# Performance work log

Hardware: AMD Instinct MI355X
Metric: run time of the kernel (lower is better)

The kernel has to match this reference:

```python
import jax, jax.numpy as jnp
import numpy as np

B, S, H, D = 1, 8192, 16, 128
BS = 64            # sparse_block_size
NB = S // BS       # 128 blocks
NUM_ORACLES = 32
ORACLE = S // NUM_ORACLES          # 256
LOCAL = ORACLE // BS               # 4 sliding-window blocks
PATTERN_ID = 0


def _build_block_pattern():
    """Block-level mask exactly as DKernelPredefinedSparseAttention.create_mask((0,))."""
    qb = np.arange(NB)[:, None]
    kb = np.arange(NB)[None, :]
    causal = qb >= kb
    window = (qb - kb) < LOCAL
    vert = np.zeros(NB, dtype=bool)
    real_col = int(PATTERN_ID * ORACLE + 0.5)
    vert[real_col // BS:(real_col + ORACLE) // BS] = True
    vert[0:1] = True
    mask = causal & (window | vert[None, :])
    kmax = int(mask.sum(axis=1).max())  # = 8 for this pattern
    kidx = np.zeros((NB, kmax), dtype=np.int32)
    kvalid = np.zeros((NB, kmax), dtype=bool)
    for i in range(NB):
        idx = np.nonzero(mask[i])[0]
        kidx[i, :len(idx)] = idx
        kvalid[i, :len(idx)] = True
    return kidx, kvalid


def setup_inputs() -> dict:
    key = jax.random.key(0)
    kq, kk, kv = jax.random.split(key, 3)
    q = jax.random.normal(kq, (B, S, H, D), dtype=jnp.float32)
    k = jax.random.normal(kk, (B, S, H, D), dtype=jnp.float32)
    v = jax.random.normal(kv, (B, S, H, D), dtype=jnp.float32)
    kidx_np, kvalid_np = _build_block_pattern()
    return {"q": q, "k": k, "v": v,
            "kidx": jnp.asarray(kidx_np), "kvalid": jnp.asarray(kvalid_np)}


def reference(q, k, v, kidx, kvalid):
    # q,k,v: [B,S,H,D] (bshd). kidx/kvalid: [NB, Kmax] active k-block ids per q-block.
    b, s, h, d = q.shape
    nb = s // BS
    kmax = kidx.shape[1]
    qb = q.reshape(b, nb, BS, h, d)
    kb = k.reshape(b, nb, BS, h, d)
    vb = v.reshape(b, nb, BS, h, d)
    # Gather only active k/v blocks -> [B, nb, Kmax, BS, H, D]
    kg = kb[:, kidx]
    vg = vb[:, kidx]
    scale = 1.0 / jnp.sqrt(jnp.float32(d))
    # [B, H, nb, BS(q), Kmax, BS(k)]
    scores = jnp.einsum('bqahd,bqkchd->bhqakc', qb, kg) * scale
    # element-level causal mask within the block pattern
    qpos = jnp.arange(nb)[:, None] * BS + jnp.arange(BS)[None, :]          # [nb, BS]
    kpos = kidx[..., None] * BS + jnp.arange(BS)[None, None, :]            # [nb, Kmax, BS]
    allow = (qpos[:, :, None, None] >= kpos[:, None, :, :]) & kvalid[:, None, :, None]
    scores = jnp.where(allow[None, None], scores, jnp.float32(-1e30))
    probs = jax.nn.softmax(scores.reshape(b, h, nb, BS, kmax * BS), axis=-1)
    probs = probs.reshape(scores.shape)
    out = jnp.einsum('bhqakc,bqkchd->bqahd', probs, vg)
    return out.reshape(b, s, h, d)
```

## Files before the change

### kernel.cpp

```cpp
#include <hip/hip_runtime.h>
#include <hip/hip_bf16.h>

#define HH 16
#define DD 128
#define NBQ 128
#define SS 8192

typedef __attribute__((ext_vector_type(4))) float f32x4;
typedef __attribute__((ext_vector_type(4))) short bf16x4;
typedef __attribute__((ext_vector_type(8))) short bf16x8;

__device__ __forceinline__ short f2bf_hw(float f) {
  __hip_bfloat16 b = __float2bfloat16(f);
  return __builtin_bit_cast(short, b);
}

__device__ __forceinline__ void gload_lds16(const void* g, void* l) {
  __builtin_amdgcn_global_load_lds(
      (const __attribute__((address_space(1))) void*)g,
      (__attribute__((address_space(3))) void*)l, 16, 0, 0);
}

__global__ __launch_bounds__(256)
void conv_vt2_kernel(const float* __restrict__ vg, unsigned short* __restrict__ vt) {
  __shared__ unsigned short tile[128 * 72];
  const int kb = blockIdx.x, h = blockIdx.y, tid = threadIdx.x;
  {
    const int r = tid >> 2, q = tid & 3;
    const float* vp = vg + ((size_t)(kb * 64 + r) * HH + h) * DD + q * 32;
    #pragma unroll
    for (int c = 0; c < 8; ++c) {
      f32x4 a = *(const f32x4*)(vp + c * 4);
      #pragma unroll
      for (int j = 0; j < 4; ++j)
        tile[(q * 32 + c * 4 + j) * 72 + r] = (unsigned short)f2bf_hw(a[j]);
    }
  }
  __syncthreads();
  const int d = tid >> 1, half = tid & 1;
  unsigned short* op = vt + ((size_t)(h * NBQ + kb) * 128 + d) * 64 + half * 32;
  #pragma unroll
  for (int j = 0; j < 4; ++j) {
    bf16x8 f;
    #pragma unroll
    for (int e = 0; e < 8; ++e) {
      const int p = half * 32 + j * 8 + e;
      const int key = ((p >> 2) & 3) * 16 + (p >> 4) * 4 + (p & 3);
      f[e] = (short)tile[d * 72 + key];
    }
    *(bf16x8*)(op + j * 8) = f;
  }
}

#define SWK(o) ((o) ^ ((((o) >> 8) & 7) << 4))
#define SWV(o) ((o) ^ ((((o) >> 7) & 7) << 4))

__global__ __launch_bounds__(512, 2)
void sparse_attn_v18(const float* __restrict__ qg_, const float* __restrict__ kg,
                     const unsigned short* __restrict__ vtbuf, float* __restrict__ outg) {
  extern __shared__ __align__(16) char lds[];

  const int bx   = blockIdx.x;
  const int w    = (bx & 7) * 128 + (bx >> 3);
  const int h    = w >> 6;
  const int qgrp = w & 63;
  const int tid  = threadIdx.x;
  const int wid  = tid >> 6;
  const int lane = tid & 63;
  const int l15  = lane & 15;
  const int lg   = lane >> 4;

  const int qlo  = qgrp * 2, qhi = qgrp * 2 + 1;
  const int qb_w = qlo + (wid >> 2);
  const int rib0 = (wid & 3) * 16;

  const int nv     = (qhi + 1 < 4) ? qhi + 1 : 4;
  const int wstart = (qlo - 3 > 4) ? qlo - 3 : 4;
  const int nw     = (qhi - wstart + 1 > 0) ? qhi - wstart + 1 : 0;
  const int nlist  = nv + nw;

  const float scale = 0.12752030522080552f;

  const int rowg = qgrp * 128 + (wid >> 2) * 64 + rib0;

  bf16x8 qa[4];
  {
    const float* qp = qg_ + ((size_t)(rowg + l15) * HH + h) * DD;
    #pragma unroll
    for (int kc = 0; kc < 4; ++kc) {
      const int d0 = kc * 32 + lg * 8;
      f32x4 a = *(const f32x4*)(qp + d0);
      f32x4 b = *(const f32x4*)(qp + d0 + 4);
      bf16x8 f;
      f[0] = f2bf_hw(a[0] * scale); f[1] = f2bf_hw(a[1] * scale);
      f[2] = f2bf_hw(a[2] * scale); f[3] = f2bf_hw(a[3] * scale);
      f[4] = f2bf_hw(b[0] * scale); f[5] = f2bf_hw(b[1] * scale);
      f[6] = f2bf_hw(b[2] * scale); f[7] = f2bf_hw(b[3] * scale);
      qa[kc] = f;
    }
  }

  f32x4 oa[8];
  #pragma unroll
  for (int i = 0; i < 8; ++i) oa[i] = (f32x4){0.f, 0.f, 0.f, 0.f};
  float mr = -1e30f;
  float lr = 0.f;

  const int kkey = tid >> 3;
  const int kd0  = (tid & 7) * 16;
  const int kob0 = SWK(tid * 32);
  const int kob1 = SWK(tid * 32 + 16);
  const char* vbase = (const char*)vtbuf + ((size_t)h * NBQ << 14);
  const int vo0 = wid * 1024 + lane * 16;

  {
    const float* kp = kg + (((size_t)(0 * 64 + kkey)) * HH + h) * DD + kd0;
    f32x4 ka = *(const f32x4*)(kp);
    f32x4 kb_ = *(const f32x4*)(kp + 4);
    f32x4 kc = *(const f32x4*)(kp + 8);
    f32x4 kd = *(const f32x4*)(kp + 12);
    bf16x8 w0, w1;
    w0[0] = f2bf_hw(ka[0]); w0[1] = f2bf_hw(ka[1]); w0[2] = f2bf_hw(ka[2]); w0[3] = f2bf_hw(ka[3]);
    w0[4] = f2bf_hw(kb_[0]); w0[5] = f2bf_hw(kb_[1]); w0[6] = f2bf_hw(kb_[2]); w0[7] = f2bf_hw(kb_[3]);
    w1[0] = f2bf_hw(kc[0]); w1[1] = f2bf_hw(kc[1]); w1[2] = f2bf_hw(kc[2]); w1[3] = f2bf_hw(kc[3]);
    w1[4] = f2bf_hw(kd[0]); w1[5] = f2bf_hw(kd[1]); w1[6] = f2bf_hw(kd[2]); w1[7] = f2bf_hw(kd[3]);
    *(bf16x8*)(lds + kob0) = w0;
    *(bf16x8*)(lds + kob1) = w1;
    #pragma unroll
    for (int p = 0; p < 2; ++p) {
      const int o = p * 8192 + vo0;
      gload_lds16(vbase + SWV(o), lds + 32768 + p * 8192 + wid * 1024);
    }
  }
  __syncthreads();

  for (int t = 0; t < nlist; ++t) {
    const int kb = (t < nv) ? t : (wstart + (t - nv));
    const bool valid = (kb <= qb_w) && ((qb_w - kb < 4) || (kb < 4));
    char* Kb = lds + (t & 1) * 16384;
    char* Vb = lds + 32768 + (t & 1) * 16384;
    const bool havenext = (t + 1 < nlist);
    const int kbn = havenext ? ((t + 1 < nv) ? (t + 1) : (wstart + (t + 1 - nv))) : 0;

    f32x4 ks0, ks1, ks2, ks3;
    if (havenext) {
      const float* kp = kg + (((size_t)(kbn * 64 + kkey)) * HH + h) * DD + kd0;
      ks0 = *(const f32x4*)(kp);
      ks1 = *(const f32x4*)(kp + 4);
      ks2 = *(const f32x4*)(kp + 8);
      ks3 = *(const f32x4*)(kp + 12);
      const char* vsrc = vbase + ((size_t)kbn << 14);
      char* Vd = lds + 32768 + ((t + 1) & 1) * 16384;
      #pragma unroll
      for (int p = 0; p < 2; ++p) {
        const int o = p * 8192 + vo0;
        gload_lds16(vsrc + SWV(o), Vd + p * 8192 + wid * 1024);
      }
    }

    f32x4 s[4];
    if (valid) {
      #pragma unroll
      for (int kt = 0; kt < 4; ++kt) s[kt] = (f32x4){0.f, 0.f, 0.f, 0.f};
      __builtin_amdgcn_s_setprio(1);
      #pragma unroll
      for (int kt = 0; kt < 4; ++kt) {
        const int key = kt * 16 + l15;
        #pragma unroll
        for (int kc = 0; kc < 4; ++kc) {
          const int off = (key * 256 + (kc * 32 + lg * 8) * 2) ^ ((key & 7) << 4);
          bf16x8 kf = *(const bf16x8*)(Kb + off);
          s[kt] = __builtin_amdgcn_mfma_f32_16x16x32_bf16(kf, qa[kc], s[kt], 0, 0, 0);
        }
      }
      __builtin_amdgcn_s_setprio(0);
    }

    if (havenext) {
      char* Kd = lds + ((t + 1) & 1) * 16384;
      bf16x8 w0, w1;
      w0[0] = f2bf_hw(ks0[0]); w0[1] = f2bf_hw(ks0[1]); w0[2] = f2bf_hw(ks0[2]); w0[3] = f2bf_hw(ks0[3]);
      w0[4] = f2bf_hw(ks1[0]); w0[5] = f2bf_hw(ks1[1]); w0[6] = f2bf_hw(ks1[2]); w0[7] = f2bf_hw(ks1[3]);
      w1[0] = f2bf_hw(ks2[0]); w1[1] = f2bf_hw(ks2[1]); w1[2] = f2bf_hw(ks2[2]); w1[3] = f2bf_hw(ks2[3]);
      w1[4] = f2bf_hw(ks3[0]); w1[5] = f2bf_hw(ks3[1]); w1[6] = f2bf_hw(ks3[2]); w1[7] = f2bf_hw(ks3[3]);
      *(bf16x8*)(Kd + kob0) = w0;
      *(bf16x8*)(Kd + kob1) = w1;
    }

    if (valid) {
      if (kb == qb_w) {
        const int rib = rib0 + l15;
        #pragma unroll
        for (int kt = 0; kt < 4; ++kt)
          #pragma unroll
          for (int r = 0; r < 4; ++r) {
            const int key = kt * 16 + lg * 4 + r;
            if (rib < key) s[kt][r] = -1e30f;
          }
      }

      {
        float a0 = fmaxf(fmaxf(s[0][0], s[0][1]), fmaxf(s[0][2], s[0][3]));
        float a1 = fmaxf(fmaxf(s[1][0], s[1][1]), fmaxf(s[1][2], s[1][3]));
        float a2 = fmaxf(fmaxf(s[2][0], s[2][1]), fmaxf(s[2][2], s[2][3]));
        float a3 = fmaxf(fmaxf(s[3][0], s[3][1]), fmaxf(s[3][2], s[3][3]));
        float lanemax = fmaxf(fmaxf(a0, a1), fmaxf(a2, a3));
        if (!__all(lanemax <= mr + 8.f)) {
          float mx = lanemax;
          mx = fmaxf(mx, __shfl_xor(mx, 16));
          mx = fmaxf(mx, __shfl_xor(mx, 32));
          const float mnew = fmaxf(mr, mx);
          const float sc = __builtin_amdgcn_exp2f(mr - mnew);
          lr *= sc;
          mr = mnew;
          const float s0 = __shfl(sc, lg * 4 + 0);
          const float s1 = __shfl(sc, lg * 4 + 1);
          const float s2 = __shfl(sc, lg * 4 + 2);
          const float s3 = __shfl(sc, lg * 4 + 3);
          #pragma unroll
          for (int nd = 0; nd < 8; ++nd) {
            oa[nd][0] *= s0; oa[nd][1] *= s1;
            oa[nd][2] *= s2; oa[nd][3] *= s3;
          }
        }
        float lsum = 0.f;
        #pragma unroll
        for (int kt = 0; kt < 4; ++kt)
          #pragma unroll
          for (int r = 0; r < 4; ++r) {
            const float p = __builtin_amdgcn_exp2f(s[kt][r] - mr);
            s[kt][r] = p;
            lsum += p;
          }
        lr += lsum;
      }

      bf16x4 pa[4];
      #pragma unroll
      for (int kt = 0; kt < 4; ++kt) {
        unsigned u0 = (unsigned)(unsigned short)f2bf_hw(s[kt][0]) |
                      ((unsigned)(unsigned short)f2bf_hw(s[kt][1]) << 16);
        unsigned u1 = (unsigned)(unsigned short)f2bf_hw(s[kt][2]) |
                      ((unsigned)(unsigned short)f2bf_hw(s[kt][3]) << 16);
        uint2 uu; uu.x = u0; uu.y = u1;
        pa[kt] = __builtin_bit_cast(bf16x4, uu);
      }

      __builtin_amdgcn_s_setprio(1);
      #pragma unroll
      for (int nd = 0; nd < 8; ++nd) {
        const int d = nd * 16 + l15;
        #pragma unroll
        for (int hb = 0; hb < 2; ++hb) {
          const int off = (d * 128 + lg * 32 + hb * 16) ^ ((d & 7) << 4);
          bf16x8 v2 = *(const bf16x8*)(Vb + off);
          bf16x4 vlo = __builtin_shufflevector(v2, v2, 0, 1, 2, 3);
          bf16x4 vhi = __builtin_shufflevector(v2, v2, 4, 5, 6, 7);
          oa[nd] = __builtin_amdgcn_mfma_f32_16x16x16bf16_1k(pa[2 * hb],     vlo, oa[nd], 0, 0, 0);
          oa[nd] = __builtin_amdgcn_mfma_f32_16x16x16bf16_1k(pa[2 * hb + 1], vhi, oa[nd], 0, 0, 0);
        }
      }
      __builtin_amdgcn_s_setprio(0);
    }
    __syncthreads();
  }

  {
    float l = lr;
    l += __shfl_xor(l, 16);
    l += __shfl_xor(l, 32);
    const float inv = 1.0f / l;
    const float i0 = __shfl(inv, lg * 4 + 0);
    const float i1 = __shfl(inv, lg * 4 + 1);
    const float i2 = __shfl(inv, lg * 4 + 2);
    const float i3 = __shfl(inv, lg * 4 + 3);
    float* op = outg + ((size_t)rowg * HH + h) * DD;
    #pragma unroll
    for (int nd = 0; nd < 8; ++nd) {
      const int d = nd * 16 + l15;
      op[(size_t)(lg * 4 + 0) * HH * DD + d] = oa[nd][0] * i0;
      op[(size_t)(lg * 4 + 1) * HH * DD + d] = oa[nd][1] * i1;
      op[(size_t)(lg * 4 + 2) * HH * DD + d] = oa[nd][2] * i2;
      op[(size_t)(lg * 4 + 3) * HH * DD + d] = oa[nd][3] * i3;
    }
  }
}

extern "C" void kernel_launch(void* const* d_in, const int* in_sizes, int n_in,
                              void* d_out, int out_size, void* d_ws, size_t ws_size,
                              hipStream_t stream) {
  const float* q = (const float*)d_in[0];
  const float* k = (const float*)d_in[1];
  const float* v = (const float*)d_in[2];
  float* out = (float*)d_out;
  unsigned short* vtbuf = (unsigned short*)d_ws;

  conv_vt2_kernel<<<dim3(NBQ, HH), 256, 0, stream>>>(v, vtbuf);
  sparse_attn_v18<<<dim3(NBQ / 2 * HH), 512, 65536, stream>>>(q, k, vtbuf, out);
}
```

Measured before the change: 119.0 us.

## Prefetch K two blocks ahead and replace syncthreads with counted waitcnt barrier

K global loads are now issued two iterations ahead and held in registers, so their latency spans a whole iteration instead of being waited on right away. The end-of-loop __syncthreads is replaced by a top-of-loop s_waitcnt vmcnt(4) plus a raw s_barrier. This lets the outstanding K register loads stay in flight while the V direct-to-LDS loads for the current buffer are confirmed complete. The hand-counted vmcnt depends on the exact number of outstanding loads, which could race if the compiler reorders or splits the memory operations.

```diff
diff --git a/kernel.cpp b/kernel.cpp
--- a/kernel.cpp
+++ b/kernel.cpp
@@ -19,6 +19,12 @@
   __builtin_amdgcn_global_load_lds(
       (const __attribute__((address_space(1))) void*)g,
       (__attribute__((address_space(3))) void*)l, 16, 0, 0);
+}
+
+__device__ __forceinline__ void wg_barrier() {
+  asm volatile("" ::: "memory");
+  __builtin_amdgcn_s_barrier();
+  asm volatile("" ::: "memory");
 }
 
 __global__ __launch_bounds__(256)
@@ -56,7 +62,7 @@
 #define SWV(o) ((o) ^ ((((o) >> 7) & 7) << 4))
 
 __global__ __launch_bounds__(512, 2)
-void sparse_attn_v18(const float* __restrict__ qg_, const float* __restrict__ kg,
+void sparse_attn_v21(const float* __restrict__ qg_, const float* __restrict__ kg,
                      const unsigned short* __restrict__ vtbuf, float* __restrict__ outg) {
   extern __shared__ __align__(16) char lds[];
 
@@ -106,33 +112,43 @@
   float mr = -1e30f;
   float lr = 0.f;
 
+  const char* vbase = (const char*)vtbuf + ((size_t)h * NBQ << 14);
+  const int o0 = wid * 1024 + lane * 16;
+
   const int kkey = tid >> 3;
   const int kd0  = (tid & 7) * 16;
   const int kob0 = SWK(tid * 32);
   const int kob1 = SWK(tid * 32 + 16);
-  const char* vbase = (const char*)vtbuf + ((size_t)h * NBQ << 14);
-  const int vo0 = wid * 1024 + lane * 16;
+  const float* ksrc0 = kg + (((size_t)kkey) * HH + h) * DD + kd0;
+  const size_t kblkstride = (size_t)64 * HH * DD;
+
+  f32x4 ks0, ks1, ks2, ks3;
 
   {
-    const float* kp = kg + (((size_t)(0 * 64 + kkey)) * HH + h) * DD + kd0;
-    f32x4 ka = *(const f32x4*)(kp);
-    f32x4 kb_ = *(const f32x4*)(kp + 4);
-    f32x4 kc = *(const f32x4*)(kp + 8);
-    f32x4 kd = *(const f32x4*)(kp + 12);
+    const float* kp = ksrc0;
+    f32x4 a0 = *(const f32x4*)(kp);
+    f32x4 a1 = *(const f32x4*)(kp + 4);
+    f32x4 a2 = *(const f32x4*)(kp + 8);
+    f32x4 a3 = *(const f32x4*)(kp + 12);
+    #pragma unroll
+    for (int p = 0; p < 2; ++p) {
+      const int o = p * 8192 + o0;
+      gload_lds16(vbase + SWV(o), lds + 32768 + p * 8192 + wid * 1024);
+    }
     bf16x8 w0, w1;
-    w0[0] = f2bf_hw(ka[0]); w0[1] = f2bf_hw(ka[1]); w0[2] = f2bf_hw(ka[2]); w0[3] = f2bf_hw(ka[3]);
-    w0[4] = f2bf_hw(kb_[0]); w0[5] = f2bf_hw(kb_[1]); w0[6] = f2bf_hw(kb_[2]); w0[7] = f2bf_hw(kb_[3]);
-    w1[0] = f2bf_hw(kc[0]); w1[1] = f2bf_hw(kc[1]); w1[2] = f2bf_hw(kc[2]); w1[3] = f2bf_hw(kc[3]);
-    w1[4] = f2bf_hw(kd[0]); w1[5] = f2bf_hw(kd[1]); w1[6] = f2bf_hw(kd[2]); w1[7] = f2bf_hw(kd[3]);
+    w0[0] = f2bf_hw(a0[0]); w0[1] = f2bf_hw(a0[1]); w0[2] = f2bf_hw(a0[2]); w0[3] = f2bf_hw(a0[3]);
+    w0[4] = f2bf_hw(a1[0]); w0[5] = f2bf_hw(a1[1]); w0[6] = f2bf_hw(a1[2]); w0[7] = f2bf_hw(a1[3]);
+    w1[0] = f2bf_hw(a2[0]); w1[1] = f2bf_hw(a2[1]); w1[2] = f2bf_hw(a2[2]); w1[3] = f2bf_hw(a2[3]);
+    w1[4] = f2bf_hw(a3[0]); w1[5] = f2bf_hw(a3[1]); w1[6] = f2bf_hw(a3[2]); w1[7] = f2bf_hw(a3[3]);
     *(bf16x8*)(lds + kob0) = w0;
     *(bf16x8*)(lds + kob1) = w1;
-    #pragma unroll
-    for (int p = 0; p < 2; ++p) {
-      const int o = p * 8192 + vo0;
-      gload_lds16(vbase + SWV(o), lds + 32768 + p * 8192 + wid * 1024);
-    }
-  }
-  __syncthreads();
+    const int kb1 = (1 < nv) ? 1 : wstart;
+    const float* kp1 = ksrc0 + (size_t)kb1 * kblkstride;
+    ks0 = *(const f32x4*)(kp1);
+    ks1 = *(const f32x4*)(kp1 + 4);
+    ks2 = *(const f32x4*)(kp1 + 8);
+    ks3 = *(const f32x4*)(kp1 + 12);
+  }
 
   for (int t = 0; t < nlist; ++t) {
     const int kb = (t < nv) ? t : (wstart + (t - nv));
@@ -140,20 +156,21 @@
     char* Kb = lds + (t & 1) * 16384;
     char* Vb = lds + 32768 + (t & 1) * 16384;
     const bool havenext = (t + 1 < nlist);
-    const int kbn = havenext ? ((t + 1 < nv) ? (t + 1) : (wstart + (t + 1 - nv))) : 0;
-
-    f32x4 ks0, ks1, ks2, ks3;
+
     if (havenext) {
-      const float* kp = kg + (((size_t)(kbn * 64 + kkey)) * HH + h) * DD + kd0;
-      ks0 = *(const f32x4*)(kp);
-      ks1 = *(const f32x4*)(kp + 4);
-      ks2 = *(const f32x4*)(kp + 8);
-      ks3 = *(const f32x4*)(kp + 12);
+      asm volatile("s_waitcnt vmcnt(4) lgkmcnt(0)" ::: "memory");
+    } else {
+      asm volatile("s_waitcnt vmcnt(0) lgkmcnt(0)" ::: "memory");
+    }
+    wg_barrier();
+
+    if (havenext) {
+      const int kbn = (t + 1 < nv) ? (t + 1) : (wstart + (t + 1 - nv));
       const char* vsrc = vbase + ((size_t)kbn << 14);
       char* Vd = lds + 32768 + ((t + 1) & 1) * 16384;
       #pragma unroll
       for (int p = 0; p < 2; ++p) {
-        const int o = p * 8192 + vo0;
+        const int o = p * 8192 + o0;
         gload_lds16(vsrc + SWV(o), Vd + p * 8192 + wid * 1024);
       }
     }
@@ -185,6 +202,14 @@
       w1[4] = f2bf_hw(ks3[0]); w1[5] = f2bf_hw(ks3[1]); w1[6] = f2bf_hw(ks3[2]); w1[7] = f2bf_hw(ks3[3]);
       *(bf16x8*)(Kd + kob0) = w0;
       *(bf16x8*)(Kd + kob1) = w1;
+      if (t + 2 < nlist) {
+        const int kb2 = (t + 2 < nv) ? (t + 2) : (wstart + (t + 2 - nv));
+        const float* kp2 = ksrc0 + (size_t)kb2 * kblkstride;
+        ks0 = *(const f32x4*)(kp2);
+        ks1 = *(const f32x4*)(kp2 + 4);
+        ks2 = *(const f32x4*)(kp2 + 8);
+        ks3 = *(const f32x4*)(kp2 + 12);
+      }
     }
 
     if (valid) {
@@ -262,7 +287,6 @@
       }
       __builtin_amdgcn_s_setprio(0);
     }
-    __syncthreads();
   }
 
   {
@@ -296,5 +320,5 @@
   unsigned short* vtbuf = (unsigned short*)d_ws;
 
   conv_vt2_kernel<<<dim3(NBQ, HH), 256, 0, stream>>>(v, vtbuf);
-  sparse_attn_v18<<<dim3(NBQ / 2 * HH), 512, 65536, stream>>>(q, k, vtbuf, out);
-}
+  sparse_attn_v21<<<dim3(NBQ / 2 * HH), 512, 65536, stream>>>(q, k, vtbuf, out);
+}
```

Result: faster. 108.7 us (-8.6%).
